# Optimization experiments

Hardware: AMD Instinct MI355X
Metric: run time of the kernel (lower is better)

Reference implementation:

```python
import jax, jax.numpy as jnp
import numpy as np


def setup_inputs() -> dict:
    key = jax.random.key(0)
    k1, k2 = jax.random.split(key)
    bz, c, h, w = 8, 512, 64, 64
    x = jax.random.normal(k1, (bz, c, h, w), dtype=jnp.float32)
    # binary mask over spatial positions; flag is its flattened view (must be consistent)
    mask = jax.random.randint(k2, (h, w), 0, 2, dtype=jnp.int32)
    flag = mask.reshape(-1)
    return {"input": x, "mask": mask, "flag": flag,
            "shift_sz": 1, "stride": 1, "triple_w": 1}


def reference(input, mask, flag, shift_sz, stride, triple_w):
    # input: [B, C, H, W]; former = first C/2 channels (decoder feats),
    # latter = last C/2 channels (encoder feats). shift_sz=stride=1 -> 1x1 patches,
    # i.e. per-pixel feature vectors.
    bz, c, h, w = input.shape
    ch = c // 2
    S = h * w
    former = input[:, :ch]                      # [B, ch, H, W]
    latter = input[:, ch:]                      # [B, ch, H, W]

    f = former.reshape(bz, ch, S).transpose(0, 2, 1)   # [B, S, ch] query pixels
    l = latter.reshape(bz, ch, S).transpose(0, 2, 1)   # [B, S, ch] key pixels

    # _norm: L2-normalize latter patches (rows)
    l_norm = l / jnp.maximum(jnp.linalg.norm(l, axis=-1, keepdims=True), 1e-12)

    # cosine-style similarity between every former pixel and every latter pixel
    sim = jnp.einsum('bqc,bkc->bqk', f, l_norm)        # [B, S, S]

    # only non-masked (flag==0) latter pixels are valid match candidates
    neg = jnp.asarray(-1e30, sim.dtype)
    sim = jnp.where((flag == 0)[None, None, :], sim, neg)
    idx = jnp.argmax(sim, axis=-1)                     # [B, S] nearest-neighbor index

    # gather matched latter pixels; paste only at masked (flag==1) positions,
    # zero elsewhere (masked_fill_(inv_ex_mask, 0) zeroes the non-mask region)
    shifted = jnp.take_along_axis(l, idx[..., None], axis=1)       # [B, S, ch]
    shifted = jnp.where((flag == 1)[None, :, None], shifted, 0.0)
    shifted = shifted.transpose(0, 2, 1).reshape(bz, ch, h, w)

    return jnp.concatenate([former, latter, shifted], axis=1)       # [B, 3*ch, H, W]
```

## Files before the change

### kernel.cpp

```cpp
#include <hip/hip_runtime.h>

#define S    4096
#define CH   256
#define NB   8

#define BM   64
#define BN   64
#define KSPLIT 8

#define SFF  256.0f
#define SLL  1024.0f

#define NEG_INF (-3.402823466e38f)

typedef _Float16 half8 __attribute__((ext_vector_type(8)));
typedef float    f32x4 __attribute__((ext_vector_type(4)));

__global__ void compact(const int* __restrict__ flag, int* __restrict__ cnts,
                        int* __restrict__ qlist, int* __restrict__ klist,
                        int* __restrict__ qpos,  int* __restrict__ kpos) {
    __shared__ int sq[256], sk[256];
    int t = threadIdx.x;
    int base = t * 16;
    int f[16];
    int nq = 0, nk = 0;
    #pragma unroll
    for (int i = 0; i < 16; ++i) {
        f[i] = flag[base + i];
        nq += (f[i] == 1);
        nk += (f[i] == 0);
    }
    sq[t] = nq; sk[t] = nk;
    __syncthreads();
    for (int off = 1; off < 256; off <<= 1) {
        int vq = sq[t], vk = sk[t];
        int aq = (t >= off) ? sq[t - off] : 0;
        int ak = (t >= off) ? sk[t - off] : 0;
        __syncthreads();
        sq[t] = vq + aq; sk[t] = vk + ak;
        __syncthreads();
    }
    int pq = sq[t] - nq;
    int pk = sk[t] - nk;
    #pragma unroll
    for (int i = 0; i < 16; ++i) {
        if (f[i] == 1) { qpos[base + i] = pq; qlist[pq++] = base + i; }
        else           { kpos[base + i] = pk; klist[pk++] = base + i; }
    }
    if (t == 255) { cnts[0] = sq[255]; cnts[1] = sk[255]; }
}

__global__ void pack_both(const float* __restrict__ x, const int* __restrict__ flag,
                          const int* __restrict__ qpos, const int* __restrict__ kpos,
                          float* __restrict__ out) {
    __shared__ float T[16][257];
    const int b = blockIdx.z;
    const int t = threadIdx.x;
    const int s = blockIdx.x * 256 + t;

    if (blockIdx.y < 4) {
        const int c0b = blockIdx.y * 64;
        const float* src = x + (size_t)b * 512 * S + blockIdx.x * 256;
        const bool active = (flag[s] == 1);
        const int row = active ? qpos[s] : 0;
        half8* F2 = (half8*)(out + (size_t)b * 768 * S);
        const int g  = row >> 4;
        const int sr = row & 15;
        for (int c0 = c0b; c0 < c0b + 64; c0 += 16) {
            #pragma unroll
            for (int i = 0; i < 16; ++i)
                T[i][t] = src[(size_t)(c0 + i) * S + t];
            __syncthreads();
            if (active) {
                #pragma unroll
                for (int g8 = 0; g8 < 2; ++g8) {
                    const int c  = c0 + g8 * 8;
                    const int cc = c >> 5;
                    const int l4 = (c >> 3) & 3;
                    half8 hb, lb;
                    #pragma unroll
                    for (int j = 0; j < 8; ++j) {
                        float v = T[g8 * 8 + j][t] * SFF;
                        _Float16 h = (_Float16)v;
                        hb[j] = h;
                        lb[j] = (_Float16)(v - (float)h);
                    }
                    F2[(size_t)(((g * 2 + 0) * 8 + cc) * 64) + sr * 4 + l4] = hb;
                    F2[(size_t)(((g * 2 + 1) * 8 + cc) * 64) + sr * 4 + l4] = lb;
                }
            }
            __syncthreads();
        }
    } else {
        const float* src = x + ((size_t)b * 512 + 256) * S + blockIdx.x * 256;
        const bool active = (flag[s] == 0);
        const int row = active ? kpos[s] : 0;
        _Float16* LH = (_Float16*)(out + (size_t)b * 768 * S) + 2 * (size_t)S * CH;
        _Float16* LL = LH + (size_t)S * CH;

        float acc = 0.f;
        for (int c0 = 0; c0 < CH; c0 += 16) {
            #pragma unroll
            for (int i = 0; i < 16; ++i)
                T[i][t] = src[(size_t)(c0 + i) * S + t];
            __syncthreads();
            #pragma unroll
            for (int i = 0; i < 16; ++i) {
                float v = T[i][t];
                acc += v * v;
            }
            __syncthreads();
        }
        const float w = active ? (1.0f / fmaxf(sqrtf(acc), 1e-12f)) * SLL : 0.f;

        for (int c0 = 0; c0 < CH; c0 += 16) {
            #pragma unroll
            for (int i = 0; i < 16; ++i)
                T[i][t] = src[(size_t)(c0 + i) * S + t];
            __syncthreads();
            if (active) {
                #pragma unroll
                for (int g8 = 0; g8 < 2; ++g8) {
                    union { _Float16 u[8]; float4 v; } hb, lb;
                    #pragma unroll
                    for (int j = 0; j < 8; ++j) {
                        float v = T[g8 * 8 + j][t] * w;
                        _Float16 h = (_Float16)v;
                        hb.u[j] = h;
                        lb.u[j] = (_Float16)(v - (float)h);
                    }
                    *(float4*)&LH[(size_t)row * CH + c0 + g8 * 8] = hb.v;
                    *(float4*)&LL[(size_t)row * CH + c0 + g8 * 8] = lb.v;
                }
            }
            __syncthreads();
        }
    }
}

__global__ void zero_pad(const int* __restrict__ cnts, float* __restrict__ out) {
    const int b  = blockIdx.y;
    const int Aq = cnts[0], Ak = cnts[1];
    const int aqp = (Aq + BM - 1) & ~(BM - 1);
    const int akp = (Ak + BN - 1) & ~(BN - 1);
    _Float16* pb = (_Float16*)(out + (size_t)b * 768 * S);
    int i = blockIdx.x * 256 + threadIdx.x;
    half8 z = { 0, 0, 0, 0, 0, 0, 0, 0 };
    if (i < 8192) {
        int p = i >> 12, rem = i & 4095;
        int row = Aq + (rem >> 5);
        int sl  = rem & 31;
        if (row < aqp) {
            half8* F2 = (half8*)pb;
            F2[(size_t)((((row >> 4) * 2 + p) * 8 + (sl >> 2)) * 64) + (row & 15) * 4 + (sl & 3)] = z;
        }
    } else {
        int j = i - 8192, panel = j >> 11, jdx = j & 2047;
        int row = Ak + (jdx >> 5);
        if (row < akp)
            *(half8*)(pb + (size_t)(2 + panel) * S * CH + (size_t)row * CH + (jdx & 31) * 8) = z;
    }
}

#define MFMA(A, B, C) __builtin_amdgcn_mfma_f32_16x16x32_f16((A), (B), (C), 0, 0, 0)

#define GLDS(SRC, OFF) __builtin_amdgcn_global_load_lds( \
    (const __attribute__((address_space(1))) void*)(SRC), \
    (__attribute__((address_space(3))) void*)(lds + (OFF)), 16, 0, 0)

#define STAGE(OFF) do { GLDS(s4, (OFF) + woff); GLDS(s5, (OFF) + 4096 + woff); } while (0)

#define ADV() do { \
    if (tn + 1 < nchunk) { \
        if ((tn & 7) == 7) { s4 += 32320; s5 += 32320; } \
        else               { s4 += 64;    s5 += 64;    } \
    } \
    ++tn; \
} while (0)

#define FOLD() do { \
    _Pragma("unroll") \
    for (int nt = 0; nt < 4; ++nt) { \
        int kp = kpb + nt * 16; \
        if (kp < Ak) { \
            _Pragma("unroll") \
            for (int r = 0; r < 4; ++r) { \
                float sv = acc[nt][r]; \
                if (sv > rm[r]) { rm[r] = sv; ri[r] = kp; } \
            } \
        } \
        acc[nt] = (f32x4){0.f, 0.f, 0.f, 0.f}; \
    } \
    kpb += 64; \
} while (0)

#define CBODY(BASE, CC) do { \
    const char* _bh = lds + (BASE) + boff0h; \
    const char* _bl = lds + (BASE) + boff0l; \
    half8 bh0 = *(const half8*)(_bh); \
    half8 bl0 = *(const half8*)(_bl); \
    half8 bh1 = *(const half8*)(_bh + 2048); \
    half8 bl1 = *(const half8*)(_bl + 2048); \
    half8 bh2 = *(const half8*)(_bh + 4096); \
    half8 bl2 = *(const half8*)(_bl + 4096); \
    half8 bh3 = *(const half8*)(_bh + 6144); \
    half8 bl3 = *(const half8*)(_bl + 6144); \
    acc[0] = MFMA(ah[CC], bh0, acc[0]); \
    acc[1] = MFMA(ah[CC], bh1, acc[1]); \
    acc[2] = MFMA(ah[CC], bh2, acc[2]); \
    acc[3] = MFMA(ah[CC], bh3, acc[3]); \
    acc[0] = MFMA(ah[CC], bl0, acc[0]); \
    acc[1] = MFMA(ah[CC], bl1, acc[1]); \
    acc[2] = MFMA(ah[CC], bl2, acc[2]); \
    acc[3] = MFMA(ah[CC], bl3, acc[3]); \
    acc[0] = MFMA(al[CC], bh0, acc[0]); \
    acc[1] = MFMA(al[CC], bh1, acc[1]); \
    acc[2] = MFMA(al[CC], bh2, acc[2]); \
    acc[3] = MFMA(al[CC], bh3, acc[3]); \
} while (0)

#define ITER(TL, BUFL, NXL) do { \
    asm volatile("s_waitcnt vmcnt(4)" ::: "memory"); \
    __builtin_amdgcn_s_barrier(); \
    STAGE(NXL); ADV(); \
    __builtin_amdgcn_s_setprio(1); \
    CBODY(BUFL, TL); \
    __builtin_amdgcn_s_setprio(0); \
    if (((TL) & 7) == 7) FOLD(); \
} while (0)

__launch_bounds__(256)
__global__ void argmax_mfma(const float* __restrict__ outbuf,
                            const int*  __restrict__ cnts,
                            float* __restrict__ pmax,
                            int*   __restrict__ pidx) {
    __shared__ __align__(1024) char lds[4 * 8192];

    const int Aq    = cnts[0];
    const int Ak    = cnts[1];
    const int b     = blockIdx.y;
    const int split = blockIdx.x & (KSPLIT - 1);
    const int q0    = (blockIdx.x >> 3) * BM;
    if (q0 >= Aq) return;

    const int tid  = threadIdx.x;
    const int lane = tid & 63;
    const int wid  = tid >> 6;
    const int l15  = lane & 15;
    const int l4   = lane >> 4;
    const int woff = wid * 1024;

    const _Float16* pb  = (const _Float16*)(outbuf + (size_t)b * 768 * S);
    const _Float16* LHg = pb + 2 * (size_t)S * CH;
    const _Float16* LLg = pb + 3 * (size_t)S * CH;

    const int nkt = (Ak + BN - 1) / BN;
    const int kt0 = (nkt * split) / KSPLIT;
    const int kt1 = (nkt * (split + 1)) / KSPLIT;
    const int nchunk = (kt1 - kt0) * 8;

    float rm[4]; int ri[4];
    #pragma unroll
    for (int i = 0; i < 4; ++i) { rm[i] = NEG_INF; ri[i] = 0; }

    const int boff0h = l15 * 128 + ((l4 * 16) ^ ((l15 & 7) << 4));
    const int boff0l = boff0h ^ 64;

    if (nchunk > 0) {
        half8 ah[8], al[8];
        {
            const half8* F2 = (const half8*)pb;
            const int g0 = (q0 >> 4) + wid;
            const int lo = l15 * 4 + l4;
            #pragma unroll
            for (int cc = 0; cc < 8; ++cc) {
                ah[cc] = F2[(size_t)(((g0 * 2 + 0) * 8 + cc) * 64) + lo];
                al[cc] = F2[(size_t)(((g0 * 2 + 1) * 8 + cc) * 64) + lo];
            }
        }

        const char *s4, *s5;
        {
            #define LSRC(P) ({ int s_ = (P) * 256 + tid; int row_ = s_ >> 3; \
                int ls_ = (s_ & 7) ^ (row_ & 7); \
                (const char*)(((ls_ < 4) ? LHg : LLg) + (size_t)(kt0 * BN + row_) * CH + (ls_ & 3) * 8); })
            s4 = LSRC(0); s5 = LSRC(1);
            #undef LSRC
        }
        int tn = 0;

        f32x4 acc[4];
        #pragma unroll
        for (int nt = 0; nt < 4; ++nt) acc[nt] = (f32x4){0.f, 0.f, 0.f, 0.f};

        int kpb = kt0 * BN + l15;

        STAGE(0);     ADV();
        STAGE(8192);  ADV();
        STAGE(16384); ADV();

        for (int t = 0; t < nchunk; t += 8) {
            ITER(0, 0,     24576);
            ITER(1, 8192,  0);
            ITER(2, 16384, 8192);
            ITER(3, 24576, 16384);
            ITER(4, 0,     24576);
            ITER(5, 8192,  0);
            ITER(6, 16384, 8192);
            ITER(7, 24576, 16384);
        }
    }

    #pragma unroll
    for (int r = 0; r < 4; ++r) {
        float m = rm[r]; int id = ri[r];
        #pragma unroll
        for (int off = 8; off; off >>= 1) {
            float om = __shfl_xor(m, off, 64);
            int   oi = __shfl_xor(id, off, 64);
            if (om > m || (om == m && oi < id)) { m = om; id = oi; }
        }
        if (l15 == 0) {
            int qp = q0 + wid * 16 + l4 * 4 + r;
            if (qp < Aq) {
                size_t o = ((size_t)((b << 12) + qp)) * KSPLIT + split;
                pmax[o] = m;
                pidx[o] = id;
            }
        }
    }
}

__global__ void combine(const int* __restrict__ cnts, const int* __restrict__ qlist,
                        const int* __restrict__ klist,
                        const float* __restrict__ pmax, const int* __restrict__ pidx,
                        int* __restrict__ idxb) {
    int qp = blockIdx.x * 256 + threadIdx.x;
    int b  = blockIdx.y;
    if (qp >= cnts[0]) return;
    size_t base = (size_t)((b << 12) + qp) * KSPLIT;
    float m = pmax[base]; int id = pidx[base];
    #pragma unroll
    for (int s = 1; s < KSPLIT; ++s) {
        float om = pmax[base + s]; int oi = pidx[base + s];
        if (om > m) { m = om; id = oi; }
    }
    idxb[((size_t)b << 12) + qlist[qp]] = klist[id];
}

__global__ void writeback(const float* __restrict__ x, const int* __restrict__ flag,
                          const int* __restrict__ idxb, float* __restrict__ out) {
    int i = blockIdx.x * 256 + threadIdx.x;
    int b = blockIdx.y;
    int c = i >> 10;
    float4* dst = (float4*)(out + (size_t)b * 768 * S) + i;
    if (c < 512) {
        *dst = ((const float4*)(x + (size_t)b * 512 * S))[i];
    } else {
        const float* src = x + ((size_t)b * 512 + 256 + (c - 512)) * S;
        const int* ib = idxb + ((size_t)b << 12);
        int q = (i & 1023) * 4;
        float4 v = { 0.f, 0.f, 0.f, 0.f };
        if (flag[q + 0] == 1) v.x = src[ib[q + 0]];
        if (flag[q + 1] == 1) v.y = src[ib[q + 1]];
        if (flag[q + 2] == 1) v.z = src[ib[q + 2]];
        if (flag[q + 3] == 1) v.w = src[ib[q + 3]];
        *dst = v;
    }
}

extern "C" void kernel_launch(void* const* d_in, const int* in_sizes, int n_in,
                              void* d_out, int out_size, void* d_ws, size_t ws_size,
                              hipStream_t stream) {
    const float* x    = (const float*)d_in[0];
    const int*   flag = (const int*)d_in[2];
    float*       out  = (float*)d_out;

    char* ws = (char*)d_ws;
    int*   cnts  = (int*)(ws);
    int*   qlist = (int*)(ws + 1024);
    int*   klist = (int*)(ws + 17408);
    int*   qpos  = (int*)(ws + 33792);
    int*   kpos  = (int*)(ws + 50176);
    int*   idxb  = (int*)(ws + 66560);
    float* pmax  = (float*)(ws + 197632);
    int*   pidx  = (int*)(ws + 1246208);

    hipLaunchKernelGGL(compact,     dim3(1),                     dim3(256), 0, stream, flag, cnts, qlist, klist, qpos, kpos);
    hipLaunchKernelGGL(pack_both,   dim3(S / 256, 5, NB),        dim3(256), 0, stream, x, flag, qpos, kpos, out);
    hipLaunchKernelGGL(zero_pad,    dim3(48, NB),                dim3(256), 0, stream, cnts, out);
    hipLaunchKernelGGL(argmax_mfma, dim3((S / BM) * KSPLIT, NB), dim3(256), 0, stream, out, cnts, pmax, pidx);
    hipLaunchKernelGGL(combine,     dim3(S / 256, NB),           dim3(256), 0, stream, cnts, qlist, klist, pmax, pidx, idxb);
    hipLaunchKernelGGL(writeback,   dim3(768 * 1024 / 256, NB),  dim3(256), 0, stream, x, flag, idxb, out);
}
```

Measured before the change: 158.1 us.

## Double query rows per wave to reuse LDS key fragments across two M-tiles

Raises the query tile from 64 to 128 rows, so each wave now holds two 16-row query fragments in registers and reuses every LDS-loaded key fragment for two MFMA chains. This halves the LDS reads and the global key traffic per unit of work. The cost is doubled accumulator and A-fragment register use, which can lower occupancy, and half as many blocks in the grid.

```diff
diff --git a/kernel.cpp b/kernel.cpp
--- a/kernel.cpp
+++ b/kernel.cpp
@@ -4,7 +4,7 @@
 #define CH   256
 #define NB   8
 
-#define BM   64
+#define BM   128
 #define BN   64
 #define KSPLIT 8
 
@@ -184,39 +184,37 @@
         int kp = kpb + nt * 16; \
         if (kp < Ak) { \
             _Pragma("unroll") \
-            for (int r = 0; r < 4; ++r) { \
-                float sv = acc[nt][r]; \
-                if (sv > rm[r]) { rm[r] = sv; ri[r] = kp; } \
+            for (int mt = 0; mt < 2; ++mt) { \
+                _Pragma("unroll") \
+                for (int r = 0; r < 4; ++r) { \
+                    const int ix = mt * 4 + r; \
+                    float sv = acc[mt][nt][r]; \
+                    if (sv > rm[ix]) { rm[ix] = sv; ri[ix] = kp; } \
+                } \
             } \
         } \
-        acc[nt] = (f32x4){0.f, 0.f, 0.f, 0.f}; \
+        acc[0][nt] = (f32x4){0.f, 0.f, 0.f, 0.f}; \
+        acc[1][nt] = (f32x4){0.f, 0.f, 0.f, 0.f}; \
     } \
     kpb += 64; \
 } while (0)
 
+#define CSTEP(BASE, CC, NTOFF, N) do { \
+    half8 bh = *(const half8*)(lds + (BASE) + boff0h + (NTOFF)); \
+    half8 bl = *(const half8*)(lds + (BASE) + boff0l + (NTOFF)); \
+    acc[0][N] = MFMA(ah0[CC], bh, acc[0][N]); \
+    acc[1][N] = MFMA(ah1[CC], bh, acc[1][N]); \
+    acc[0][N] = MFMA(ah0[CC], bl, acc[0][N]); \
+    acc[1][N] = MFMA(ah1[CC], bl, acc[1][N]); \
+    acc[0][N] = MFMA(al0[CC], bh, acc[0][N]); \
+    acc[1][N] = MFMA(al1[CC], bh, acc[1][N]); \
+} while (0)
+
 #define CBODY(BASE, CC) do { \
-    const char* _bh = lds + (BASE) + boff0h; \
-    const char* _bl = lds + (BASE) + boff0l; \
-    half8 bh0 = *(const half8*)(_bh); \
-    half8 bl0 = *(const half8*)(_bl); \
-    half8 bh1 = *(const half8*)(_bh + 2048); \
-    half8 bl1 = *(const half8*)(_bl + 2048); \
-    half8 bh2 = *(const half8*)(_bh + 4096); \
-    half8 bl2 = *(const half8*)(_bl + 4096); \
-    half8 bh3 = *(const half8*)(_bh + 6144); \
-    half8 bl3 = *(const half8*)(_bl + 6144); \
-    acc[0] = MFMA(ah[CC], bh0, acc[0]); \
-    acc[1] = MFMA(ah[CC], bh1, acc[1]); \
-    acc[2] = MFMA(ah[CC], bh2, acc[2]); \
-    acc[3] = MFMA(ah[CC], bh3, acc[3]); \
-    acc[0] = MFMA(ah[CC], bl0, acc[0]); \
-    acc[1] = MFMA(ah[CC], bl1, acc[1]); \
-    acc[2] = MFMA(ah[CC], bl2, acc[2]); \
-    acc[3] = MFMA(ah[CC], bl3, acc[3]); \
-    acc[0] = MFMA(al[CC], bh0, acc[0]); \
-    acc[1] = MFMA(al[CC], bh1, acc[1]); \
-    acc[2] = MFMA(al[CC], bh2, acc[2]); \
-    acc[3] = MFMA(al[CC], bh3, acc[3]); \
+    CSTEP(BASE, CC, 0,    0); \
+    CSTEP(BASE, CC, 2048, 1); \
+    CSTEP(BASE, CC, 4096, 2); \
+    CSTEP(BASE, CC, 6144, 3); \
 } while (0)
 
 #define ITER(TL, BUFL, NXL) do { \
@@ -259,23 +257,25 @@
     const int kt1 = (nkt * (split + 1)) / KSPLIT;
     const int nchunk = (kt1 - kt0) * 8;
 
-    float rm[4]; int ri[4];
+    float rm[8]; int ri[8];
     #pragma unroll
-    for (int i = 0; i < 4; ++i) { rm[i] = NEG_INF; ri[i] = 0; }
+    for (int i = 0; i < 8; ++i) { rm[i] = NEG_INF; ri[i] = 0; }
 
     const int boff0h = l15 * 128 + ((l4 * 16) ^ ((l15 & 7) << 4));
     const int boff0l = boff0h ^ 64;
 
     if (nchunk > 0) {
-        half8 ah[8], al[8];
+        half8 ah0[8], al0[8], ah1[8], al1[8];
         {
             const half8* F2 = (const half8*)pb;
-            const int g0 = (q0 >> 4) + wid;
+            const int g0 = (q0 >> 4) + wid * 2;
             const int lo = l15 * 4 + l4;
             #pragma unroll
             for (int cc = 0; cc < 8; ++cc) {
-                ah[cc] = F2[(size_t)(((g0 * 2 + 0) * 8 + cc) * 64) + lo];
-                al[cc] = F2[(size_t)(((g0 * 2 + 1) * 8 + cc) * 64) + lo];
+                ah0[cc] = F2[(size_t)((((g0    ) * 2 + 0) * 8 + cc) * 64) + lo];
+                al0[cc] = F2[(size_t)((((g0    ) * 2 + 1) * 8 + cc) * 64) + lo];
+                ah1[cc] = F2[(size_t)((((g0 + 1) * 2 + 0) * 8 + cc) * 64) + lo];
+                al1[cc] = F2[(size_t)((((g0 + 1) * 2 + 1) * 8 + cc) * 64) + lo];
             }
         }
 
@@ -289,9 +289,11 @@
         }
         int tn = 0;
 
-        f32x4 acc[4];
+        f32x4 acc[2][4];
         #pragma unroll
-        for (int nt = 0; nt < 4; ++nt) acc[nt] = (f32x4){0.f, 0.f, 0.f, 0.f};
+        for (int mt = 0; mt < 2; ++mt)
+            #pragma unroll
+            for (int nt = 0; nt < 4; ++nt) acc[mt][nt] = (f32x4){0.f, 0.f, 0.f, 0.f};
 
         int kpb = kt0 * BN + l15;
 
@@ -312,20 +314,24 @@
     }
 
     #pragma unroll
-    for (int r = 0; r < 4; ++r) {
-        float m = rm[r]; int id = ri[r];
+    for (int mt = 0; mt < 2; ++mt) {
         #pragma unroll
-        for (int off = 8; off; off >>= 1) {
-            float om = __shfl_xor(m, off, 64);
-            int   oi = __shfl_xor(id, off, 64);
-            if (om > m || (om == m && oi < id)) { m = om; id = oi; }
-        }
-        if (l15 == 0) {
-            int qp = q0 + wid * 16 + l4 * 4 + r;
-            if (qp < Aq) {
-                size_t o = ((size_t)((b << 12) + qp)) * KSPLIT + split;
-                pmax[o] = m;
-                pidx[o] = id;
+        for (int r = 0; r < 4; ++r) {
+            const int ix = mt * 4 + r;
+            float m = rm[ix]; int id = ri[ix];
+            #pragma unroll
+            for (int off = 8; off; off >>= 1) {
+                float om = __shfl_xor(m, off, 64);
+                int   oi = __shfl_xor(id, off, 64);
+                if (om > m || (om == m && oi < id)) { m = om; id = oi; }
+            }
+            if (l15 == 0) {
+                int qp = q0 + wid * 32 + mt * 16 + l4 * 4 + r;
+                if (qp < Aq) {
+                    size_t o = ((size_t)((b << 12) + qp)) * KSPLIT + split;
+                    pmax[o] = m;
+                    pidx[o] = id;
+                }
             }
         }
     }
```

Result: slower. 164.4 us (+4.0%).

## Replace split-K combine kernel with 64-bit atomicMax and fold zero_pad into pack

Applied to the files above, without the earlier changes.

The per-split partial max/index arrays and the separate combine kernel are replaced by a packed 64-bit key (order-preserving float bits plus an inverted index) that each block reduces with atomicMax. Writeback decodes the key through qpos/klist. The padding-zero kernel is merged into pack_both as an extra grid slice, and the compact kernel now clears the atomic buffer. Together these remove two launches and the round trip through the partial arrays, at the cost of global atomic contention and serial zeroing of 32K entries in a single-block kernel.

```diff
diff --git a/kernel.cpp b/kernel.cpp
--- a/kernel.cpp
+++ b/kernel.cpp
@@ -18,9 +18,11 @@
 
 __global__ void compact(const int* __restrict__ flag, int* __restrict__ cnts,
                         int* __restrict__ qlist, int* __restrict__ klist,
-                        int* __restrict__ qpos,  int* __restrict__ kpos) {
+                        int* __restrict__ qpos,  int* __restrict__ kpos,
+                        unsigned long long* __restrict__ amax) {
     __shared__ int sq[256], sk[256];
     int t = threadIdx.x;
+    for (int i = t; i < NB * 4096; i += 256) amax[i] = 0ULL;
     int base = t * 16;
     int f[16];
     int nq = 0, nk = 0;
@@ -51,6 +53,7 @@
 }
 
 __global__ void pack_both(const float* __restrict__ x, const int* __restrict__ flag,
+                          const int* __restrict__ cnts,
                           const int* __restrict__ qpos, const int* __restrict__ kpos,
                           float* __restrict__ out) {
     __shared__ float T[16][257];
@@ -91,7 +94,7 @@
             }
             __syncthreads();
         }
-    } else {
+    } else if (blockIdx.y == 4) {
         const float* src = x + ((size_t)b * 512 + 256) * S + blockIdx.x * 256;
         const bool active = (flag[s] == 0);
         const int row = active ? kpos[s] : 0;
@@ -135,30 +138,30 @@
             }
             __syncthreads();
         }
-    }
-}
-
-__global__ void zero_pad(const int* __restrict__ cnts, float* __restrict__ out) {
-    const int b  = blockIdx.y;
-    const int Aq = cnts[0], Ak = cnts[1];
-    const int aqp = (Aq + BM - 1) & ~(BM - 1);
-    const int akp = (Ak + BN - 1) & ~(BN - 1);
-    _Float16* pb = (_Float16*)(out + (size_t)b * 768 * S);
-    int i = blockIdx.x * 256 + threadIdx.x;
-    half8 z = { 0, 0, 0, 0, 0, 0, 0, 0 };
-    if (i < 8192) {
-        int p = i >> 12, rem = i & 4095;
-        int row = Aq + (rem >> 5);
-        int sl  = rem & 31;
-        if (row < aqp) {
-            half8* F2 = (half8*)pb;
-            F2[(size_t)((((row >> 4) * 2 + p) * 8 + (sl >> 2)) * 64) + (row & 15) * 4 + (sl & 3)] = z;
-        }
     } else {
-        int j = i - 8192, panel = j >> 11, jdx = j & 2047;
-        int row = Ak + (jdx >> 5);
-        if (row < akp)
-            *(half8*)(pb + (size_t)(2 + panel) * S * CH + (size_t)row * CH + (jdx & 31) * 8) = z;
+        const int Aq = cnts[0], Ak = cnts[1];
+        const int aqp = (Aq + BM - 1) & ~(BM - 1);
+        const int akp = (Ak + BN - 1) & ~(BN - 1);
+        _Float16* pb = (_Float16*)(out + (size_t)b * 768 * S);
+        half8 z = { 0, 0, 0, 0, 0, 0, 0, 0 };
+        #pragma unroll
+        for (int it = 0; it < 3; ++it) {
+            int i = it * 4096 + blockIdx.x * 256 + t;
+            if (i < 8192) {
+                int p = i >> 12, rem = i & 4095;
+                int row = Aq + (rem >> 5);
+                int sl  = rem & 31;
+                if (row < aqp) {
+                    half8* F2 = (half8*)pb;
+                    F2[(size_t)((((row >> 4) * 2 + p) * 8 + (sl >> 2)) * 64) + (row & 15) * 4 + (sl & 3)] = z;
+                }
+            } else {
+                int j = i - 8192, panel = j >> 11, jdx = j & 2047;
+                int row = Ak + (jdx >> 5);
+                if (row < akp)
+                    *(half8*)(pb + (size_t)(2 + panel) * S * CH + (size_t)row * CH + (jdx & 31) * 8) = z;
+            }
+        }
     }
 }
 
@@ -232,8 +235,7 @@
 __launch_bounds__(256)
 __global__ void argmax_mfma(const float* __restrict__ outbuf,
                             const int*  __restrict__ cnts,
-                            float* __restrict__ pmax,
-                            int*   __restrict__ pidx) {
+                            unsigned long long* __restrict__ amax) {
     __shared__ __align__(1024) char lds[4 * 8192];
 
     const int Aq    = cnts[0];
@@ -323,33 +325,20 @@
         if (l15 == 0) {
             int qp = q0 + wid * 16 + l4 * 4 + r;
             if (qp < Aq) {
-                size_t o = ((size_t)((b << 12) + qp)) * KSPLIT + split;
-                pmax[o] = m;
-                pidx[o] = id;
-            }
-        }
-    }
-}
-
-__global__ void combine(const int* __restrict__ cnts, const int* __restrict__ qlist,
-                        const int* __restrict__ klist,
-                        const float* __restrict__ pmax, const int* __restrict__ pidx,
-                        int* __restrict__ idxb) {
-    int qp = blockIdx.x * 256 + threadIdx.x;
-    int b  = blockIdx.y;
-    if (qp >= cnts[0]) return;
-    size_t base = (size_t)((b << 12) + qp) * KSPLIT;
-    float m = pmax[base]; int id = pidx[base];
-    #pragma unroll
-    for (int s = 1; s < KSPLIT; ++s) {
-        float om = pmax[base + s]; int oi = pidx[base + s];
-        if (om > m) { m = om; id = oi; }
-    }
-    idxb[((size_t)b << 12) + qlist[qp]] = klist[id];
+                unsigned u = __float_as_uint(m);
+                u = (m >= 0.f) ? (u | 0x80000000u) : ~u;
+                unsigned long long key =
+                    ((unsigned long long)u << 32) | (unsigned)(0xFFFFFFFFu - (unsigned)id);
+                atomicMax(&amax[((size_t)b << 12) + qp], key);
+            }
+        }
+    }
 }
 
 __global__ void writeback(const float* __restrict__ x, const int* __restrict__ flag,
-                          const int* __restrict__ idxb, float* __restrict__ out) {
+                          const int* __restrict__ qpos, const int* __restrict__ klist,
+                          const unsigned long long* __restrict__ amax,
+                          float* __restrict__ out) {
     int i = blockIdx.x * 256 + threadIdx.x;
     int b = blockIdx.y;
     int c = i >> 10;
@@ -358,13 +347,20 @@
         *dst = ((const float4*)(x + (size_t)b * 512 * S))[i];
     } else {
         const float* src = x + ((size_t)b * 512 + 256 + (c - 512)) * S;
-        const int* ib = idxb + ((size_t)b << 12);
+        const unsigned long long* am = amax + ((size_t)b << 12);
         int q = (i & 1023) * 4;
         float4 v = { 0.f, 0.f, 0.f, 0.f };
-        if (flag[q + 0] == 1) v.x = src[ib[q + 0]];
-        if (flag[q + 1] == 1) v.y = src[ib[q + 1]];
-        if (flag[q + 2] == 1) v.z = src[ib[q + 2]];
-        if (flag[q + 3] == 1) v.w = src[ib[q + 3]];
+        #pragma unroll
+        for (int j = 0; j < 4; ++j) {
+            if (flag[q + j] == 1) {
+                unsigned idc = 0xFFFFFFFFu - (unsigned)(am[qpos[q + j]] & 0xFFFFFFFFu);
+                float val = src[klist[idc]];
+                if (j == 0) v.x = val;
+                else if (j == 1) v.y = val;
+                else if (j == 2) v.z = val;
+                else v.w = val;
+            }
+        }
         *dst = v;
     }
 }
@@ -382,14 +378,14 @@
     int*   klist = (int*)(ws + 17408);
     int*   qpos  = (int*)(ws + 33792);
     int*   kpos  = (int*)(ws + 50176);
-    int*   idxb  = (int*)(ws + 66560);
-    float* pmax  = (float*)(ws + 197632);
-    int*   pidx  = (int*)(ws + 1246208);
-
-    hipLaunchKernelGGL(compact,     dim3(1),                     dim3(256), 0, stream, flag, cnts, qlist, klist, qpos, kpos);
-    hipLaunchKernelGGL(pack_both,   dim3(S / 256, 5, NB),        dim3(256), 0, stream, x, flag, qpos, kpos, out);
-    hipLaunchKernelGGL(zero_pad,    dim3(48, NB),                dim3(256), 0, stream, cnts, out);
-    hipLaunchKernelGGL(argmax_mfma, dim3((S / BM) * KSPLIT, NB), dim3(256), 0, stream, out, cnts, pmax, pidx);
-    hipLaunchKernelGGL(combine,     dim3(S / 256, NB),           dim3(256), 0, stream, cnts, qlist, klist, pmax, pidx, idxb);
-    hipLaunchKernelGGL(writeback,   dim3(768 * 1024 / 256, NB),  dim3(256), 0, stream, x, flag, idxb, out);
-}
+    unsigned long long* amax = (unsigned long long*)(ws + 66560);
+
+    hipLaunchKernelGGL(compact,     dim3(1),                     dim3(256), 0, stream,
+                       flag, cnts, qlist, klist, qpos, kpos, amax);
+    hipLaunchKernelGGL(pack_both,   dim3(S / 256, 6, NB),        dim3(256), 0, stream,
+                       x, flag, cnts, qpos, kpos, out);
+    hipLaunchKernelGGL(argmax_mfma, dim3((S / BM) * KSPLIT, NB), dim3(256), 0, stream,
+                       out, cnts, amax);
+    hipLaunchKernelGGL(writeback,   dim3(768 * 1024 / 256, NB),  dim3(256), 0, stream,
+                       x, flag, qpos, klist, amax, out);
+}
```

Measured after the change: 166.7 us. +5.4%, slower.
